# Optimization experiments

Measured on AMD Instinct MI355X. Metric: run time of the kernel, lower is better.

The kernel has to match this reference:

```python
import jax, jax.numpy as jnp
import numpy as np

K = 3      # kernel size (hardcoded 3x3 in the torch module via repeat(...,9,...))
PAD = 1
STRIDE = 1


def _unfold(x):
    # torch.nn.functional.unfold equivalent: (B,C,H,W) -> (B,C,K,K,oh,ow)
    B, C, H, W = x.shape
    p = jax.lax.conv_general_dilated_patches(
        x, (K, K), (STRIDE, STRIDE), ((PAD, PAD), (PAD, PAD)))
    oh, ow = p.shape[2], p.shape[3]
    return p.reshape(B, C, K, K, oh, ow)


def setup_inputs() -> dict:
    key = jax.random.key(0)
    k1, k2, k3, k4 = jax.random.split(key, 4)
    B, Cin, Cout, H, W = 4, 64, 64, 128, 128
    inputs = jax.random.normal(k1, (B, Cin, H, W), jnp.float32)
    depth = jax.random.uniform(k2, (B, 1, H, W), jnp.float32)  # positive depths
    weight = jax.random.uniform(k3, (K, Cout, Cin, K, K), jnp.float32, minval=-0.05, maxval=0.05)
    bias = jax.random.uniform(k4, (Cout,), jnp.float32, minval=-0.05, maxval=0.05)
    return {"inputs": inputs, "depth": depth, "weight": weight, "bias": bias, "f": 1}


def reference(inputs, depth, weight, bias, f):
    # --- DepthKernelFn: per-depth-plane binary masks ---
    depth_wins = _unfold(depth)          # (B,1,K,K,oh,ow)
    s_wins = depth_wins / f              # grid spacing s_i = d / f
    cy, cx = K // 2, K // 2
    d0 = depth_wins[:, :, cy, cx]        # center depth      (B,1,oh,ow)
    s0 = s_wins[:, :, cy, cx]            # center spacing    (B,1,oh,ow)
    offs = jnp.arange(K, dtype=inputs.dtype) - (K - 1) / 2.0  # l - (K-1)/2
    # z_l at center: d0 + (l-1)*s0  -> (K,B,1,oh,ow)
    z0 = d0[None] + offs[:, None, None, None, None] * s0[None]
    half = s0[None] / 2
    a = (z0 - half)[:, :, :, None, None]  # (K,B,1,1,1,oh,ow)
    b = (z0 + half)[:, :, :, None, None]
    dw = depth_wins[None]                 # (1,B,1,K,K,oh,ow)
    # mask_l = 1 where a <= depth < b else 0  (same as the where-cascade in torch)
    mask = ((dw >= a) & (dw < b)).astype(inputs.dtype)  # (K,B,1,K,K,oh,ow)

    # --- RepeatKernelConvFn: masked windowed conv via einsum ---
    inp_wins = _unfold(inputs)            # (B,C,K,K,oh,ow)
    x = inp_wins[None] * mask             # (K,B,C,K,K,oh,ow), depth C=1 broadcasts
    out = jnp.einsum('hijklmn,hojkl->iomn', x, weight)
    out = out + bias.reshape(1, -1, 1, 1)
    return out
```

## Files before the change

kernel.cpp:

```cpp
#include <hip/hip_runtime.h>
#include <math.h>

#define B_N  4
#define CIN  64
#define COUT 64
#define H_N  128
#define W_N  128

typedef _Float16 half8 __attribute__((ext_vector_type(8)));
typedef float    f32x4 __attribute__((ext_vector_type(4)));

#define KTOT   1728
#define NSTEP  54
#define WA_BYTES ((size_t)NSTEP * 4 * 64 * 8 * 2)

__global__ void wprep(const float* __restrict__ w, _Float16* __restrict__ wa) {
    int idx = blockIdx.x * 256 + threadIdx.x;
    if (idx >= NSTEP * 4 * 64) return;
    int lane = idx & 63;
    int mt   = (idx >> 6) & 3;
    int s    = idx >> 8;
    int m    = mt * 16 + (lane & 15);
    int kl0  = (lane >> 4) * 8;
    _Float16 v[8];
#pragma unroll
    for (int j = 0; j < 8; ++j) {
        int k = s * 32 + kl0 + j;
        int g = k >> 6;
        int c = k & 63;
        int t = g / 3;
        int h = g % 3;
        v[j] = (_Float16)w[(((size_t)(h * COUT) + m) * CIN + c) * 9 + t];
    }
    *(int4*)&wa[(size_t)idx * 8] = *(int4*)v;
}

#define XS_STRIDE 72
#define XS_ROW    (130 * XS_STRIDE)

__global__ __launch_bounds__(256)
void conv_mfma(const float* __restrict__ inp, const float* __restrict__ depth,
               const _Float16* __restrict__ wa, const float* __restrict__ bias,
               const int* __restrict__ fptr, float* __restrict__ out) {
    __shared__ _Float16 Xs[3 * XS_ROW];

    int bid  = blockIdx.x;
    int y    = bid & (H_N - 1);
    int b    = bid >> 7;
    int tid  = threadIdx.x;
    int lane = tid & 63;
    int wid  = tid >> 6;
    int p0   = wid * 32;
    int ln15 = lane & 15;
    int quad = lane >> 4;

    {
        int x     = tid & 127;
        int chalf = tid >> 7;
        for (int dyi = 0; dyi < 3; ++dyi) {
            int yy = y + dyi - 1;
            _Float16 buf[32];
            if (yy >= 0 && yy < H_N) {
                const float* src = inp + (((size_t)b * CIN + chalf * 32) * H_N + yy) * W_N + x;
#pragma unroll
                for (int cc = 0; cc < 32; ++cc)
                    buf[cc] = (_Float16)src[(size_t)cc * H_N * W_N];
            } else {
#pragma unroll
                for (int cc = 0; cc < 32; ++cc) buf[cc] = (_Float16)0.f;
            }
            _Float16* dst = &Xs[dyi * XS_ROW + (x + 1) * XS_STRIDE + chalf * 32];
#pragma unroll
            for (int k = 0; k < 4; ++k)
                *(int4*)&dst[k * 8] = *(int4*)&buf[k * 8];
        }
        if (tid < 48) {
            int dyi = tid / 16;
            int rem = tid % 16;
            int xi  = (rem >= 8) ? 129 : 0;
            int k8  = rem & 7;
            int4 z  = {0, 0, 0, 0};
            *(int4*)&Xs[dyi * XS_ROW + xi * XS_STRIDE + k8 * 8] = z;
        }
    }

    double fd = (double)(*fptr);
    unsigned hpk[2];
#pragma unroll
    for (int nt = 0; nt < 2; ++nt) {
        int x = p0 + nt * 16 + ln15;
        float d0f = depth[((size_t)b * H_N + y) * W_N + x];
        double dd = (double)d0f;
        double s0 = dd / fd;
        unsigned pk = 0;
        for (int t = 0; t < 9; ++t) {
            int dy = t / 3 - 1, dx = t % 3 - 1;
            int yy = y + dy, xx = x + dx;
            float dwf = (yy >= 0 && yy < H_N && xx >= 0 && xx < W_N)
                        ? depth[((size_t)b * H_N + yy) * W_N + xx] : 0.f;
            int h = -1;
            if (s0 > 0.0) {
                double u  = ((double)dwf - dd) / s0 + 1.5;
                double uf = floor(u);
                if (uf >= 0.0 && uf <= 2.0) h = (int)uf;
            }
            pk |= (unsigned)(h + 1) << (2 * t);
        }
        hpk[nt] = pk;
    }

    __syncthreads();

    f32x4 acc[4][2];
#pragma unroll
    for (int mt = 0; mt < 4; ++mt)
#pragma unroll
        for (int nt = 0; nt < 2; ++nt) acc[mt][nt] = (f32x4){0.f, 0.f, 0.f, 0.f};

    const half8* wa8 = (const half8*)wa;

    for (int t = 0; t < 9; ++t) {
        int dyi = t / 3;
        int dx  = t % 3 - 1;
        int boff0 = dyi * XS_ROW + (p0 + 0  + ln15 + dx + 1) * XS_STRIDE + quad * 8;
        int boff1 = dyi * XS_ROW + (p0 + 16 + ln15 + dx + 1) * XS_STRIDE + quad * 8;
        int hb0 = (hpk[0] >> (2 * t)) & 3;
        int hb1 = (hpk[1] >> (2 * t)) & 3;

        half8 A[6][4];
        {
            const half8* base = wa8 + ((size_t)t * 6 * 4) * 64 + lane;
#pragma unroll
            for (int j = 0; j < 6; ++j)
#pragma unroll
                for (int mt = 0; mt < 4; ++mt)
                    A[j][mt] = base[(j * 4 + mt) * 64];
        }

#pragma unroll
        for (int h = 0; h < 3; ++h) {
            bool m0 = (hb0 == h + 1);
            bool m1 = (hb1 == h + 1);
#pragma unroll
            for (int kk = 0; kk < 2; ++kk) {
                int j = h * 2 + kk;
                half8 b0 = *(const half8*)&Xs[boff0 + kk * 32];
                half8 b1 = *(const half8*)&Xs[boff1 + kk * 32];
                half8 z  = {(_Float16)0.f, (_Float16)0.f, (_Float16)0.f, (_Float16)0.f,
                            (_Float16)0.f, (_Float16)0.f, (_Float16)0.f, (_Float16)0.f};
                b0 = m0 ? b0 : z;
                b1 = m1 ? b1 : z;
#pragma unroll
                for (int mt = 0; mt < 4; ++mt) {
                    acc[mt][0] = __builtin_amdgcn_mfma_f32_16x16x32_f16(A[j][mt], b0, acc[mt][0], 0, 0, 0);
                    acc[mt][1] = __builtin_amdgcn_mfma_f32_16x16x32_f16(A[j][mt], b1, acc[mt][1], 0, 0, 0);
                }
            }
        }
        __syncthreads();
    }

#pragma unroll
    for (int mt = 0; mt < 4; ++mt) {
#pragma unroll
        for (int nt = 0; nt < 2; ++nt) {
            int x = p0 + nt * 16 + ln15;
#pragma unroll
            for (int r = 0; r < 4; ++r) {
                int o = mt * 16 + quad * 4 + r;
                out[(((size_t)b * COUT + o) * H_N + y) * W_N + x] = acc[mt][nt][r] + bias[o];
            }
        }
    }
}

__global__ __launch_bounds__(256)
void conv25d(const float* __restrict__ inp, const float* __restrict__ depth,
             const float* __restrict__ wsrc, const float* __restrict__ bias,
             const int* __restrict__ fptr, float* __restrict__ out) {
    int bid = blockIdx.x;
    int xt  = bid & 3;
    int y   = (bid >> 2) & (H_N - 1);
    int b   = bid >> 9;
    int o   = threadIdx.x & 63;
    int q   = threadIdx.x >> 6;
    int x0  = xt * 32 + q * 8;
    double fd = (double)(*fptr);
    float acc[8];
    float bv = bias[o];
#pragma unroll
    for (int i = 0; i < 8; ++i) acc[i] = bv;
    const float* dcen = depth + ((size_t)b * H_N + y) * W_N;
    float d0[8];
#pragma unroll
    for (int i = 0; i < 8; ++i) d0[i] = dcen[x0 + i];
    for (int t = 0; t < 9; ++t) {
        int dy = t / 3 - 1, dx = t % 3 - 1;
        int yy = y + dy;
        if (yy < 0 || yy >= H_N) continue;
        const float* drow = depth + ((size_t)b * H_N + yy) * W_N;
        int hsel[8];
#pragma unroll
        for (int i = 0; i < 8; ++i) {
            int xx = x0 + i + dx;
            int h = -1;
            if (xx >= 0 && xx < W_N) {
                double dd = (double)d0[i];
                double s0 = dd / fd;
                if (s0 > 0.0) {
                    double u = ((double)drow[xx] - dd) / s0 + 1.5;
                    double uf = floor(u);
                    if (uf >= 0.0 && uf <= 2.0) h = (int)uf;
                }
            }
            hsel[i] = h;
        }
        const float* irow = inp + ((size_t)b * CIN * H_N + yy) * W_N;
        for (int c = 0; c < CIN; ++c) {
            const float* wb = wsrc + ((size_t)o * CIN + c) * 9 + t;
            float w0 = wb[0], w1 = wb[(size_t)COUT * CIN * 9], w2 = wb[2 * (size_t)COUT * CIN * 9];
            const float* ir = irow + (size_t)c * H_N * W_N;
#pragma unroll
            for (int i = 0; i < 8; ++i) {
                int h = hsel[i];
                if (h >= 0) {
                    float wv = (h == 0) ? w0 : ((h == 1) ? w1 : w2);
                    acc[i] = fmaf(ir[x0 + i + dx], wv, acc[i]);
                }
            }
        }
    }
    float* orow = out + (((size_t)b * COUT + o) * H_N + y) * W_N;
#pragma unroll
    for (int i = 0; i < 8; ++i) orow[x0 + i] = acc[i];
}

extern "C" void kernel_launch(void* const* d_in, const int* in_sizes, int n_in,
                              void* d_out, int out_size, void* d_ws, size_t ws_size,
                              hipStream_t stream) {
    const float* inp   = (const float*)d_in[0];
    const float* depth = (const float*)d_in[1];
    const float* w     = (const float*)d_in[2];
    const float* bias  = (const float*)d_in[3];
    const int*   f     = (const int*)d_in[4];
    float* out = (float*)d_out;

    if (ws_size >= WA_BYTES) {
        _Float16* wa = (_Float16*)d_ws;
        wprep<<<NSTEP, 256, 0, stream>>>(w, wa);
        conv_mfma<<<B_N * H_N, 256, 0, stream>>>(inp, depth, wa, bias, f, out);
    } else {
        conv25d<<<B_N * H_N * (W_N / 32), 256, 0, stream>>>(inp, depth, w, bias, f, out);
    }
}
```

Baseline: 106.1 us.

## Swizzle LDS input tile, hoist B loads per tap, and load A per depth plane

Replaces the padded LDS row stride (72 halves) with a 64-half line and an XOR swizzle on 16-byte chunks keyed by column, to avoid bank conflicts while using less shared memory. The four B fragments per tap are now loaded once and reused across the three depth planes, instead of being reloaded for each plane. Weight fragments are loaded per depth plane (8 half8 vectors) rather than all 24 up front, which lowers register pressure. Adds a launch-bounds hint of 3 blocks per SM. The smaller LDS footprint and fewer registers should allow higher occupancy, at the cost of exposing more global-load latency for the weights.

```diff
diff --git a/kernel.cpp b/kernel.cpp
--- a/kernel.cpp
+++ b/kernel.cpp
@@ -35,10 +35,10 @@
     *(int4*)&wa[(size_t)idx * 8] = *(int4*)v;
 }
 
-#define XS_STRIDE 72
-#define XS_ROW    (130 * XS_STRIDE)
-
-__global__ __launch_bounds__(256)
+#define XS_LINE 64
+#define XS_ROW  (130 * XS_LINE)
+
+__global__ __launch_bounds__(256, 3)
 void conv_mfma(const float* __restrict__ inp, const float* __restrict__ depth,
                const _Float16* __restrict__ wa, const float* __restrict__ bias,
                const int* __restrict__ fptr, float* __restrict__ out) {
@@ -57,6 +57,8 @@
     {
         int x     = tid & 127;
         int chalf = tid >> 7;
+        int xi    = x + 1;
+        int key   = xi & 7;
         for (int dyi = 0; dyi < 3; ++dyi) {
             int yy = y + dyi - 1;
             _Float16 buf[32];
@@ -69,18 +71,18 @@
 #pragma unroll
                 for (int cc = 0; cc < 32; ++cc) buf[cc] = (_Float16)0.f;
             }
-            _Float16* dst = &Xs[dyi * XS_ROW + (x + 1) * XS_STRIDE + chalf * 32];
+            _Float16* dst = &Xs[dyi * XS_ROW + xi * XS_LINE];
 #pragma unroll
             for (int k = 0; k < 4; ++k)
-                *(int4*)&dst[k * 8] = *(int4*)&buf[k * 8];
+                *(int4*)&dst[((chalf * 4 + k) ^ key) * 8] = *(int4*)&buf[k * 8];
         }
         if (tid < 48) {
             int dyi = tid / 16;
             int rem = tid % 16;
-            int xi  = (rem >= 8) ? 129 : 0;
+            int xz  = (rem >= 8) ? 129 : 0;
             int k8  = rem & 7;
             int4 z  = {0, 0, 0, 0};
-            *(int4*)&Xs[dyi * XS_ROW + xi * XS_STRIDE + k8 * 8] = z;
+            *(int4*)&Xs[dyi * XS_ROW + xz * XS_LINE + k8 * 8] = z;
         }
     }
 
@@ -122,38 +124,50 @@
     for (int t = 0; t < 9; ++t) {
         int dyi = t / 3;
         int dx  = t % 3 - 1;
-        int boff0 = dyi * XS_ROW + (p0 + 0  + ln15 + dx + 1) * XS_STRIDE + quad * 8;
-        int boff1 = dyi * XS_ROW + (p0 + 16 + ln15 + dx + 1) * XS_STRIDE + quad * 8;
+        int xs0 = p0 + ln15 + dx + 1;
+        int key = xs0 & 7;
+        int base0 = dyi * XS_ROW + xs0 * XS_LINE;
+        int base1 = base0 + 16 * XS_LINE;
+        int offk0 = ((quad + 0) ^ key) * 8;
+        int offk1 = ((quad + 4) ^ key) * 8;
         int hb0 = (hpk[0] >> (2 * t)) & 3;
         int hb1 = (hpk[1] >> (2 * t)) & 3;
 
-        half8 A[6][4];
-        {
-            const half8* base = wa8 + ((size_t)t * 6 * 4) * 64 + lane;
-#pragma unroll
-            for (int j = 0; j < 6; ++j)
-#pragma unroll
-                for (int mt = 0; mt < 4; ++mt)
-                    A[j][mt] = base[(j * 4 + mt) * 64];
-        }
+        half8 b00 = *(const half8*)&Xs[base0 + offk0];
+        half8 b01 = *(const half8*)&Xs[base0 + offk1];
+        half8 b10 = *(const half8*)&Xs[base1 + offk0];
+        half8 b11 = *(const half8*)&Xs[base1 + offk1];
+
+        const half8* baseA = wa8 + ((size_t)t * 6 * 4) * 64 + lane;
 
 #pragma unroll
         for (int h = 0; h < 3; ++h) {
+            half8 A0[4], A1[4];
+#pragma unroll
+            for (int mt = 0; mt < 4; ++mt) {
+                A0[mt] = baseA[(h * 8 + 0 + mt) * 64];
+                A1[mt] = baseA[(h * 8 + 4 + mt) * 64];
+            }
             bool m0 = (hb0 == h + 1);
             bool m1 = (hb1 == h + 1);
-#pragma unroll
-            for (int kk = 0; kk < 2; ++kk) {
-                int j = h * 2 + kk;
-                half8 b0 = *(const half8*)&Xs[boff0 + kk * 32];
-                half8 b1 = *(const half8*)&Xs[boff1 + kk * 32];
-                half8 z  = {(_Float16)0.f, (_Float16)0.f, (_Float16)0.f, (_Float16)0.f,
-                            (_Float16)0.f, (_Float16)0.f, (_Float16)0.f, (_Float16)0.f};
-                b0 = m0 ? b0 : z;
-                b1 = m1 ? b1 : z;
+            half8 z  = {(_Float16)0.f, (_Float16)0.f, (_Float16)0.f, (_Float16)0.f,
+                        (_Float16)0.f, (_Float16)0.f, (_Float16)0.f, (_Float16)0.f};
+            {
+                half8 c0 = m0 ? b00 : z;
+                half8 c1 = m1 ? b10 : z;
 #pragma unroll
                 for (int mt = 0; mt < 4; ++mt) {
-                    acc[mt][0] = __builtin_amdgcn_mfma_f32_16x16x32_f16(A[j][mt], b0, acc[mt][0], 0, 0, 0);
-                    acc[mt][1] = __builtin_amdgcn_mfma_f32_16x16x32_f16(A[j][mt], b1, acc[mt][1], 0, 0, 0);
+                    acc[mt][0] = __builtin_amdgcn_mfma_f32_16x16x32_f16(A0[mt], c0, acc[mt][0], 0, 0, 0);
+                    acc[mt][1] = __builtin_amdgcn_mfma_f32_16x16x32_f16(A0[mt], c1, acc[mt][1], 0, 0, 0);
+                }
+            }
+            {
+                half8 c0 = m0 ? b01 : z;
+                half8 c1 = m1 ? b11 : z;
+#pragma unroll
+                for (int mt = 0; mt < 4; ++mt) {
+                    acc[mt][0] = __builtin_amdgcn_mfma_f32_16x16x32_f16(A1[mt], c0, acc[mt][0], 0, 0, 0);
+                    acc[mt][1] = __builtin_amdgcn_mfma_f32_16x16x32_f16(A1[mt], c1, acc[mt][1], 0, 0, 0);
                 }
             }
         }
```

After: 110.6 us. +4.3%, slower.

## Swizzle LDS layout, prefetch weights and LDS fragments, batch global loads

Applied to the files above, without the earlier changes.

Replaces the padded LDS row stride with a 64-element line using an XOR swizzle to avoid bank conflicts. Weight fragments for the first tap are now loaded before the depth-mask computation, and each tap's weights and B fragments are prefetched at the end of the previous tap using double-buffered registers, with the loop fully unrolled. Input rows are loaded into registers for all three dy rows before converting and storing, and the depth division is replaced by a reciprocal multiply. Launch bounds request two blocks per SM, which raises register pressure, and the reciprocal could change mask boundaries slightly.

```diff
diff --git a/kernel.cpp b/kernel.cpp
--- a/kernel.cpp
+++ b/kernel.cpp
@@ -35,10 +35,10 @@
     *(int4*)&wa[(size_t)idx * 8] = *(int4*)v;
 }
 
-#define XS_STRIDE 72
-#define XS_ROW    (130 * XS_STRIDE)
-
-__global__ __launch_bounds__(256)
+#define XS_LINE 64
+#define XS_ROW  (130 * XS_LINE)
+
+__global__ __launch_bounds__(256, 2)
 void conv_mfma(const float* __restrict__ inp, const float* __restrict__ depth,
                const _Float16* __restrict__ wa, const float* __restrict__ bias,
                const int* __restrict__ fptr, float* __restrict__ out) {
@@ -57,32 +57,50 @@
     {
         int x     = tid & 127;
         int chalf = tid >> 7;
+        int xi    = x + 1;
+        int key   = xi & 7;
+        float fbuf[3][32];
+#pragma unroll
         for (int dyi = 0; dyi < 3; ++dyi) {
             int yy = y + dyi - 1;
-            _Float16 buf[32];
             if (yy >= 0 && yy < H_N) {
                 const float* src = inp + (((size_t)b * CIN + chalf * 32) * H_N + yy) * W_N + x;
 #pragma unroll
                 for (int cc = 0; cc < 32; ++cc)
-                    buf[cc] = (_Float16)src[(size_t)cc * H_N * W_N];
+                    fbuf[dyi][cc] = src[(size_t)cc * H_N * W_N];
             } else {
 #pragma unroll
-                for (int cc = 0; cc < 32; ++cc) buf[cc] = (_Float16)0.f;
-            }
-            _Float16* dst = &Xs[dyi * XS_ROW + (x + 1) * XS_STRIDE + chalf * 32];
+                for (int cc = 0; cc < 32; ++cc) fbuf[dyi][cc] = 0.f;
+            }
+        }
+#pragma unroll
+        for (int dyi = 0; dyi < 3; ++dyi) {
+            _Float16 hb[32];
+#pragma unroll
+            for (int cc = 0; cc < 32; ++cc) hb[cc] = (_Float16)fbuf[dyi][cc];
+            _Float16* dst = &Xs[dyi * XS_ROW + xi * XS_LINE];
 #pragma unroll
             for (int k = 0; k < 4; ++k)
-                *(int4*)&dst[k * 8] = *(int4*)&buf[k * 8];
+                *(int4*)&dst[((chalf * 4 + k) ^ key) * 8] = *(int4*)&hb[k * 8];
         }
         if (tid < 48) {
             int dyi = tid / 16;
             int rem = tid % 16;
-            int xi  = (rem >= 8) ? 129 : 0;
+            int xz  = (rem >= 8) ? 129 : 0;
             int k8  = rem & 7;
             int4 z  = {0, 0, 0, 0};
-            *(int4*)&Xs[dyi * XS_ROW + xi * XS_STRIDE + k8 * 8] = z;
-        }
-    }
+            *(int4*)&Xs[dyi * XS_ROW + xz * XS_LINE + k8 * 8] = z;
+        }
+    }
+
+    const half8* wa8   = (const half8*)wa;
+    const half8* baseA = wa8 + lane;
+    half8 A[6][4];
+#pragma unroll
+    for (int j = 0; j < 6; ++j)
+#pragma unroll
+        for (int mt = 0; mt < 4; ++mt)
+            A[j][mt] = baseA[(j * 4 + mt) * 64];
 
     double fd = (double)(*fptr);
     unsigned hpk[2];
@@ -90,8 +108,9 @@
     for (int nt = 0; nt < 2; ++nt) {
         int x = p0 + nt * 16 + ln15;
         float d0f = depth[((size_t)b * H_N + y) * W_N + x];
-        double dd = (double)d0f;
-        double s0 = dd / fd;
+        double dd  = (double)d0f;
+        double inv = fd / dd;
+        bool   pos = (inv > 0.0);
         unsigned pk = 0;
         for (int t = 0; t < 9; ++t) {
             int dy = t / 3 - 1, dx = t % 3 - 1;
@@ -99,8 +118,8 @@
             float dwf = (yy >= 0 && yy < H_N && xx >= 0 && xx < W_N)
                         ? depth[((size_t)b * H_N + yy) * W_N + xx] : 0.f;
             int h = -1;
-            if (s0 > 0.0) {
-                double u  = ((double)dwf - dd) / s0 + 1.5;
+            if (pos) {
+                double u  = ((double)dwf - dd) * inv + 1.5;
                 double uf = floor(u);
                 if (uf >= 0.0 && uf <= 2.0) h = (int)uf;
             }
@@ -117,25 +136,29 @@
 #pragma unroll
         for (int nt = 0; nt < 2; ++nt) acc[mt][nt] = (f32x4){0.f, 0.f, 0.f, 0.f};
 
-    const half8* wa8 = (const half8*)wa;
-
+    half8 bb[2][4];
+
+#define READ_B(tt) {                                                          \
+        int dyi_ = (tt) / 3; int dx_ = (tt) % 3 - 1;                          \
+        int xs0_ = p0 + ln15 + dx_ + 1;                                       \
+        int key_ = xs0_ & 7;                                                  \
+        int ba0_ = dyi_ * XS_ROW + xs0_ * XS_LINE;                            \
+        int ba1_ = ba0_ + 16 * XS_LINE;                                       \
+        bb[(tt) & 1][0] = *(const half8*)&Xs[ba0_ + ((quad    ) ^ key_) * 8]; \
+        bb[(tt) & 1][1] = *(const half8*)&Xs[ba0_ + ((quad + 4) ^ key_) * 8]; \
+        bb[(tt) & 1][2] = *(const half8*)&Xs[ba1_ + ((quad    ) ^ key_) * 8]; \
+        bb[(tt) & 1][3] = *(const half8*)&Xs[ba1_ + ((quad + 4) ^ key_) * 8]; \
+    }
+
+    READ_B(0);
+
+    half8 z8 = {(_Float16)0.f, (_Float16)0.f, (_Float16)0.f, (_Float16)0.f,
+                (_Float16)0.f, (_Float16)0.f, (_Float16)0.f, (_Float16)0.f};
+
+#pragma unroll
     for (int t = 0; t < 9; ++t) {
-        int dyi = t / 3;
-        int dx  = t % 3 - 1;
-        int boff0 = dyi * XS_ROW + (p0 + 0  + ln15 + dx + 1) * XS_STRIDE + quad * 8;
-        int boff1 = dyi * XS_ROW + (p0 + 16 + ln15 + dx + 1) * XS_STRIDE + quad * 8;
         int hb0 = (hpk[0] >> (2 * t)) & 3;
         int hb1 = (hpk[1] >> (2 * t)) & 3;
-
-        half8 A[6][4];
-        {
-            const half8* base = wa8 + ((size_t)t * 6 * 4) * 64 + lane;
-#pragma unroll
-            for (int j = 0; j < 6; ++j)
-#pragma unroll
-                for (int mt = 0; mt < 4; ++mt)
-                    A[j][mt] = base[(j * 4 + mt) * 64];
-        }
 
 #pragma unroll
         for (int h = 0; h < 3; ++h) {
@@ -143,22 +166,29 @@
             bool m1 = (hb1 == h + 1);
 #pragma unroll
             for (int kk = 0; kk < 2; ++kk) {
+                half8 c0 = m0 ? bb[t & 1][kk]     : z8;
+                half8 c1 = m1 ? bb[t & 1][2 + kk] : z8;
                 int j = h * 2 + kk;
-                half8 b0 = *(const half8*)&Xs[boff0 + kk * 32];
-                half8 b1 = *(const half8*)&Xs[boff1 + kk * 32];
-                half8 z  = {(_Float16)0.f, (_Float16)0.f, (_Float16)0.f, (_Float16)0.f,
-                            (_Float16)0.f, (_Float16)0.f, (_Float16)0.f, (_Float16)0.f};
-                b0 = m0 ? b0 : z;
-                b1 = m1 ? b1 : z;
 #pragma unroll
                 for (int mt = 0; mt < 4; ++mt) {
-                    acc[mt][0] = __builtin_amdgcn_mfma_f32_16x16x32_f16(A[j][mt], b0, acc[mt][0], 0, 0, 0);
-                    acc[mt][1] = __builtin_amdgcn_mfma_f32_16x16x32_f16(A[j][mt], b1, acc[mt][1], 0, 0, 0);
+                    acc[mt][0] = __builtin_amdgcn_mfma_f32_16x16x32_f16(A[j][mt], c0, acc[mt][0], 0, 0, 0);
+                    acc[mt][1] = __builtin_amdgcn_mfma_f32_16x16x32_f16(A[j][mt], c1, acc[mt][1], 0, 0, 0);
                 }
             }
         }
-        __syncthreads();
-    }
+
+        if (t < 8) {
+            const half8* bA = baseA + (size_t)(t + 1) * 24 * 64;
+#pragma unroll
+            for (int j = 0; j < 6; ++j)
+#pragma unroll
+                for (int mt = 0; mt < 4; ++mt)
+                    A[j][mt] = bA[(j * 4 + mt) * 64];
+            READ_B(t + 1);
+            __syncthreads();
+        }
+    }
+#undef READ_B
 
 #pragma unroll
     for (int mt = 0; mt < 4; ++mt) {
```

Result: faster. 103.9 us (-2.1%).
